# Kernel tuning notes

Hardware: AMD Instinct MI355X
Metric: run time of the kernel (lower is better)

Reference implementation:

```python
import jax, jax.numpy as jnp
import numpy as np
import math

E = 256      # emb_size
H = 4        # num_heads
D = E // H   # head_dim
EXPLORE_SCALE = 0.5
EXPLOIT_SCALE = 0.5
TEMP_MIN = 0.5
TEMP_MAX = 2.0


def setup_inputs() -> dict:
    key = jax.random.key(0)
    ks = jax.random.split(key, 12)
    B, S = 4, 2048
    his_emb = jax.random.normal(ks[0], (B, S, E), dtype=jnp.float32)
    src_key_padding_mask = jax.random.randint(ks[1], (B, S), 0, 2) > 0
    explore = jax.random.uniform(ks[2], (B, S), dtype=jnp.float32)
    exploit = jax.random.uniform(ks[3], (B, S), dtype=jnp.float32)
    scale = 1.0 / math.sqrt(E)
    Wq = jax.random.normal(ks[4], (E, E), dtype=jnp.float32) * scale
    bq = jnp.zeros((E,), dtype=jnp.float32)
    Wk = jax.random.normal(ks[5], (E, E), dtype=jnp.float32) * scale
    bk = jnp.zeros((E,), dtype=jnp.float32)
    Wv = jax.random.normal(ks[6], (E, E), dtype=jnp.float32) * scale
    bv = jnp.zeros((E,), dtype=jnp.float32)
    Wo = jax.random.normal(ks[7], (E, E), dtype=jnp.float32) * scale
    bo = jnp.zeros((E,), dtype=jnp.float32)
    return {"his_emb": his_emb, "src_key_padding_mask": src_key_padding_mask,
            "explore": explore, "exploit": exploit,
            "Wq": Wq, "bq": bq, "Wk": Wk, "bk": bk,
            "Wv": Wv, "bv": bv, "Wo": Wo, "bo": bo}


def reference(his_emb, src_key_padding_mask, explore, exploit,
              Wq, bq, Wk, bk, Wv, bv, Wo, bo):
    B, S, _ = his_emb.shape
    # projections -> [B, H, S, D]
    q = (his_emb @ Wq + bq).reshape(B, S, H, D).transpose(0, 2, 1, 3)
    k = (his_emb @ Wk + bk).reshape(B, S, H, D).transpose(0, 2, 1, 3)
    v = (his_emb @ Wv + bv).reshape(B, S, H, D).transpose(0, 2, 1, 3)
    logits = jnp.einsum('bhqd,bhkd->bhqk', q, k) / math.sqrt(D)
    attn_mask = src_key_padding_mask[:, None, None, :]  # [B,1,1,S] over keys
    logits = jnp.where(attn_mask, -1e16, logits)
    # per-query dynamic temperature
    temp = 1.0 + EXPLORE_SCALE * explore - EXPLOIT_SCALE * exploit  # [B,S]
    temp = jnp.clip(temp, TEMP_MIN, TEMP_MAX)
    temp = jnp.where(src_key_padding_mask, 1.0, temp)
    logits = logits / temp[:, None, :, None]
    probs = jax.nn.softmax(logits, axis=-1)
    probs = jnp.where(attn_mask, 0.0, probs)
    probs = probs / jnp.maximum(probs.sum(axis=-1, keepdims=True), 1e-8)
    out = jnp.einsum('bhqk,bhkd->bhqd', probs, v)
    out = out.transpose(0, 2, 1, 3).reshape(B, S, E)
    out = out @ Wo + bo
    return jnp.where(src_key_padding_mask[:, :, None], 0.0, out)
```

## Files before the change

kernel.cpp:

```cpp
#include <hip/hip_runtime.h>
#include <hip/hip_bf16.h>
#include <math.h>

#define B_ 4
#define S_ 2048
#define E_ 256
#define H_ 4
#define D_ 64
#define NROW (B_*S_)
#define NCH 4
#define CHK (S_/NCH)
#define FM 12.0f

typedef __attribute__((ext_vector_type(8))) short short8;
typedef __attribute__((ext_vector_type(4))) float floatx4;

__device__ __forceinline__ short f2bf(float f){
    union{float f; unsigned u;} x; x.f = f;
    unsigned r = x.u + 0x7fffu + ((x.u>>16)&1u);
    return (short)(r>>16);
}
__device__ __forceinline__ float bf2f(short s){
    union{unsigned u; float f;} x; x.u = ((unsigned)(unsigned short)s)<<16; return x.f;
}
__device__ __forceinline__ unsigned pk_trunc(float lo, float hi){
    return __builtin_amdgcn_perm(__float_as_uint(hi), __float_as_uint(lo), 0x07060302u);
}

__global__ __launch_bounds__(256) void convert_x(const float* __restrict__ X, short* __restrict__ Xb){
    int gid = blockIdx.x*256 + threadIdx.x;
    const float4* p = (const float4*)(X + (size_t)gid*8);
    float4 a = p[0], b = p[1];
    short8 o;
    o[0]=f2bf(a.x); o[1]=f2bf(a.y); o[2]=f2bf(a.z); o[3]=f2bf(a.w);
    o[4]=f2bf(b.x); o[5]=f2bf(b.y); o[6]=f2bf(b.z); o[7]=f2bf(b.w);
    *(short8*)(Xb + (size_t)gid*8) = o;
}

__global__ __launch_bounds__(256) void transpose_w(
    const float* __restrict__ W0, const float* __restrict__ W1,
    const float* __restrict__ W2, const float* __restrict__ W3,
    short* __restrict__ T0, short* __restrict__ T1,
    short* __restrict__ T2, short* __restrict__ T3)
{
    const float* W = blockIdx.y==0?W0: blockIdx.y==1?W1: blockIdx.y==2?W2:W3;
    short*       T = blockIdx.y==0?T0: blockIdx.y==1?T1: blockIdx.y==2?T2:T3;
    __shared__ float L[64][65];
    const int t = threadIdx.x;
    const int k0 = (blockIdx.x>>2)*64, n0 = (blockIdx.x&3)*64;
    {
        int r = t>>2, c0 = (t&3)*16;
        const float4* p = (const float4*)(W + (size_t)(k0+r)*E_ + n0 + c0);
        #pragma unroll
        for (int j=0;j<4;++j){
            float4 u = p[j];
            L[r][c0+4*j]=u.x; L[r][c0+4*j+1]=u.y; L[r][c0+4*j+2]=u.z; L[r][c0+4*j+3]=u.w;
        }
    }
    __syncthreads();
    {
        int n = t>>2, kk0 = (t&3)*16;
        short8 o0, o1;
        #pragma unroll
        for(int j=0;j<8;++j) o0[j] = f2bf(L[kk0+j][n]);
        #pragma unroll
        for(int j=0;j<8;++j) o1[j] = f2bf(L[kk0+8+j][n]);
        short* dst = T + (size_t)(n0+n)*E_ + k0 + kk0;
        *(short8*)dst = o0; *(short8*)(dst+8) = o1;
    }
}

__global__ __launch_bounds__(256) void qkv_gemm(
    const short* __restrict__ Xb,
    const short* __restrict__ Wtq, const float* __restrict__ bq,
    const short* __restrict__ Wtk, const float* __restrict__ bk,
    const short* __restrict__ Wtv, const float* __restrict__ bv,
    const int* __restrict__ mask,
    const float* __restrict__ explore, const float* __restrict__ exploit,
    short* __restrict__ Q, short* __restrict__ K, short* __restrict__ Vt)
{
    const int z = blockIdx.z;
    const short* Wt   = z==0?Wtq: z==1?Wtk:Wtv;
    const float* bias = z==0?bq:  z==1?bk:bv;

    __shared__ __align__(16) short As[64][72];
    __shared__ __align__(16) short Bs[64][72];

    const int t=threadIdx.x, w=t>>6, lane=t&63, ln=lane&15, quad=lane>>4;
    const int m0 = blockIdx.y*64, n0 = blockIdx.x*64;

    floatx4 acc[4] = {};
    for (int kt=0; kt<E_; kt+=64){
        __syncthreads();
        {
            int r=t>>2, c0=(t&3)*16;
            const uint4* pa = (const uint4*)(Xb + (size_t)(m0+r)*E_ + kt + c0);
            *(uint4*)&As[r][c0] = pa[0]; *(uint4*)&As[r][c0+8] = pa[1];
            const uint4* pb = (const uint4*)(Wt + (size_t)(n0+r)*E_ + kt + c0);
            *(uint4*)&Bs[r][c0] = pb[0]; *(uint4*)&Bs[r][c0+8] = pb[1];
        }
        __syncthreads();
        short8 a0 = *(const short8*)&As[w*16+ln][quad*8];
        short8 a1 = *(const short8*)&As[w*16+ln][32+quad*8];
        #pragma unroll
        for (int c=0;c<4;++c){
            short8 b0 = *(const short8*)&Bs[c*16+ln][quad*8];
            short8 b1 = *(const short8*)&Bs[c*16+ln][32+quad*8];
            acc[c] = __builtin_amdgcn_mfma_f32_16x16x32_bf16(a0,b0,acc[c],0,0,0);
            acc[c] = __builtin_amdgcn_mfma_f32_16x16x32_bf16(a1,b1,acc[c],0,0,0);
        }
    }
    if (z==0){
        float tscr[4];
        #pragma unroll
        for(int reg=0;reg<4;++reg){
            int row = m0 + w*16 + quad*4 + reg;
            float ex = explore[row], xp = exploit[row];
            float tmp = fminf(fmaxf(1.0f + 0.5f*ex - 0.5f*xp, 0.5f), 2.0f);
            tscr[reg] = mask[row] ? 0.125f : 1.0f/(8.0f*tmp);
        }
        #pragma unroll
        for(int c=0;c<4;++c){
            int colg = n0 + c*16 + ln;
            float bia = bias[colg];
            #pragma unroll
            for(int reg=0;reg<4;++reg){
                int row = m0 + w*16 + quad*4 + reg;
                Q[(size_t)row*E_ + colg] = f2bf((acc[c][reg] + bia)*tscr[reg]);
            }
        }
    } else if (z==1){
        #pragma unroll
        for(int c=0;c<4;++c){
            int colg = n0 + c*16 + ln;
            float bia = bias[colg];
            #pragma unroll
            for(int reg=0;reg<4;++reg){
                int row = m0 + w*16 + quad*4 + reg;
                K[(size_t)row*E_ + colg] = f2bf(acc[c][reg] + bia);
            }
        }
    } else {
        #pragma unroll
        for(int c=0;c<4;++c){
            int colg = n0 + c*16 + ln;
            int hx = colg>>6, d = colg&63;
            float bia = bias[colg];
            #pragma unroll
            for(int reg=0;reg<4;++reg){
                int row = m0 + w*16 + quad*4 + reg;
                int bb = row>>11, s = row&(S_-1);
                Vt[((size_t)((bb*H_+hx)*D_+d))*S_ + s] = f2bf(acc[c][reg] + bia);
            }
        }
    }
}

__global__ __launch_bounds__(256,4) void attn_mfma(
    const short* __restrict__ Qb, const short* __restrict__ Kb, const short* __restrict__ Vtb,
    const int* __restrict__ mask,
    short* __restrict__ OP, float* __restrict__ Lb)
{
    const int bh = blockIdx.z;
    const int b = bh>>2, h = bh&3;
    const int q0 = blockIdx.x*128;
    const int ck = blockIdx.y, k0 = ck*CHK;
    const int t=threadIdx.x, w=t>>6, lane=t&63, ln=lane&15, quad=lane>>4;

    __shared__ __align__(16) short Ks[64*64];
    __shared__ __align__(16) short Ps[4][32][72];
    __shared__ float mv[64];

    short8 qa[2][2];
    #pragma unroll
    for (int qh=0; qh<2; ++qh){
        const short* qr = Qb + (size_t)(b*S_ + q0 + w*32 + qh*16 + ln)*E_ + h*D_;
        qa[qh][0] = *(const short8*)(qr + quad*8);
        qa[qh][1] = *(const short8*)(qr + 32 + quad*8);
    }

    const int sr = t>>2, scc = (t&3)*2;
    short* kst0 = &Ks[sr*64 + ((scc  )^(sr&7))*8];
    short* kst1 = &Ks[sr*64 + ((scc+1)^(sr&7))*8];
    const short* kgl = Kb + (size_t)(b*S_ + sr)*E_ + h*D_ + scc*8;

    floatx4 of[2][4] = {};
    float lacc[2] = {0.f, 0.f};

    for (int kt=k0; kt<k0+CHK; kt+=64){
        __syncthreads();
        {
            const uint4* g = (const uint4*)(kgl + (size_t)kt*E_);
            *(uint4*)kst0 = g[0];
            *(uint4*)kst1 = g[1];
        }
        if (t<64) mv[t] = (mask[b*S_+kt+t] ? -1e30f : 0.0f) - FM;
        __syncthreads();

        #pragma unroll
        for (int c=0;c<4;++c){
            short8 ka0 = *(const short8*)&Ks[(c*16+ln)*64 + ((quad  )^(ln&7))*8];
            short8 ka1 = *(const short8*)&Ks[(c*16+ln)*64 + ((4+quad)^(ln&7))*8];
            float4 mvv = *(const float4*)&mv[c*16+quad*4];
            #pragma unroll
            for (int qh=0; qh<2; ++qh){
                floatx4 s = {};
                s = __builtin_amdgcn_mfma_f32_16x16x32_bf16(ka0, qa[qh][0], s, 0,0,0);
                s = __builtin_amdgcn_mfma_f32_16x16x32_bf16(ka1, qa[qh][1], s, 0,0,0);
                float p0 = __expf(s[0] + mvv.x);
                float p1 = __expf(s[1] + mvv.y);
                float p2 = __expf(s[2] + mvv.z);
                float p3 = __expf(s[3] + mvv.w);
                lacc[qh] += (p0+p1)+(p2+p3);
                uint2 pw; pw.x = pk_trunc(p0,p1); pw.y = pk_trunc(p2,p3);
                *(uint2*)&Ps[w][qh*16+ln][c*16+quad*4] = pw;
            }
        }

        #pragma unroll
        for (int half=0; half<2; ++half){
            short8 pa0 = *(const short8*)&Ps[w][ln]   [half*32 + quad*8];
            short8 pa1 = *(const short8*)&Ps[w][16+ln][half*32 + quad*8];
            #pragma unroll
            for (int dc=0; dc<4; ++dc){
                short8 vb = *(const short8*)(Vtb + ((size_t)(bh*D_ + dc*16+ln))*S_ + kt + half*32 + quad*8);
                of[0][dc] = __builtin_amdgcn_mfma_f32_16x16x32_bf16(pa0, vb, of[0][dc], 0,0,0);
                of[1][dc] = __builtin_amdgcn_mfma_f32_16x16x32_bf16(pa1, vb, of[1][dc], 0,0,0);
            }
        }
    }

    #pragma unroll
    for (int qh=0; qh<2; ++qh){
        float l = lacc[qh];
        l += __shfl_xor(l, 16);
        l += __shfl_xor(l, 32);
        #pragma unroll
        for (int dc=0; dc<4; ++dc){
            #pragma unroll
            for (int reg=0; reg<4; ++reg){
                int q = q0 + w*32 + qh*16 + quad*4 + reg;
                OP[((size_t)(ck*16 + bh)*S_ + q)*D_ + dc*16 + ln] = f2bf(of[qh][dc][reg]);
            }
        }
        if (quad==0)
            Lb[(size_t)(ck*16 + bh)*S_ + q0 + w*32 + qh*16 + ln] = l;
    }
}

__global__ __launch_bounds__(256) void combine(
    const short* __restrict__ OP, const float* __restrict__ Lb, short* __restrict__ CTXb)
{
    int gid = blockIdx.x*256 + threadIdx.x;
    #pragma unroll
    for (int i=0;i<4;++i){
        int idx = gid + i*524288;
        int e = idx & 255, row = idx >> 8;
        int bb = row >> 11, s = row & (S_-1);
        int hh = e >> 6, d = e & 63;
        int bh = bb*H_ + hh;
        float o = 0.f, l = 0.f;
        #pragma unroll
        for (int c=0;c<NCH;++c){
            o += bf2f(OP[((size_t)(c*16 + bh)*S_ + s)*D_ + d]);
            l += Lb[(size_t)(c*16 + bh)*S_ + s];
        }
        CTXb[idx] = f2bf(o / fmaxf(l, 1e-8f));
    }
}

__global__ __launch_bounds__(256) void out_gemm(
    const short* __restrict__ Ab, const short* __restrict__ Wto, const float* __restrict__ bo,
    const int* __restrict__ mask, float* __restrict__ out)
{
    __shared__ __align__(16) short As[64][72];
    __shared__ __align__(16) short Bs[64][72];
    const int t=threadIdx.x, w=t>>6, lane=t&63, ln=lane&15, quad=lane>>4;
    const int m0 = blockIdx.y*64, n0 = blockIdx.x*64;
    floatx4 acc[4] = {};
    for (int kt=0; kt<E_; kt+=64){
        __syncthreads();
        {
            int r=t>>2, c0=(t&3)*16;
            const uint4* pa = (const uint4*)(Ab + (size_t)(m0+r)*E_ + kt + c0);
            *(uint4*)&As[r][c0] = pa[0]; *(uint4*)&As[r][c0+8] = pa[1];
            const uint4* pb = (const uint4*)(Wto + (size_t)(n0+r)*E_ + kt + c0);
            *(uint4*)&Bs[r][c0] = pb[0]; *(uint4*)&Bs[r][c0+8] = pb[1];
        }
        __syncthreads();
        short8 a0 = *(const short8*)&As[w*16+ln][quad*8];
        short8 a1 = *(const short8*)&As[w*16+ln][32+quad*8];
        #pragma unroll
        for (int c=0;c<4;++c){
            short8 b0 = *(const short8*)&Bs[c*16+ln][quad*8];
            short8 b1 = *(const short8*)&Bs[c*16+ln][32+quad*8];
            acc[c] = __builtin_amdgcn_mfma_f32_16x16x32_bf16(a0,b0,acc[c],0,0,0);
            acc[c] = __builtin_amdgcn_mfma_f32_16x16x32_bf16(a1,b1,acc[c],0,0,0);
        }
    }
    #pragma unroll
    for(int c=0;c<4;++c){
        int colg = n0 + c*16 + ln;
        float bia = bo[colg];
        #pragma unroll
        for(int reg=0;reg<4;++reg){
            int row = m0 + w*16 + quad*4 + reg;
            out[(size_t)row*E_ + colg] = mask[row] ? 0.0f : (acc[c][reg] + bia);
        }
    }
}

extern "C" void kernel_launch(void* const* d_in, const int* in_sizes, int n_in,
                              void* d_out, int out_size, void* d_ws, size_t ws_size,
                              hipStream_t stream) {
    const float* his     = (const float*)d_in[0];
    const int*   mask    = (const int*)d_in[1];
    const float* explore = (const float*)d_in[2];
    const float* exploit = (const float*)d_in[3];
    const float* Wq = (const float*)d_in[4];
    const float* bq = (const float*)d_in[5];
    const float* Wk = (const float*)d_in[6];
    const float* bk = (const float*)d_in[7];
    const float* Wv = (const float*)d_in[8];
    const float* bv = (const float*)d_in[9];
    const float* Wo = (const float*)d_in[10];
    const float* bo = (const float*)d_in[11];

    char* ws = (char*)d_ws;
    const size_t NE2 = (size_t)NROW * E_ * 2;
    short* Wtq  = (short*)(ws);                    ws += E_*E_*2;
    short* Wtk  = (short*)(ws);                    ws += E_*E_*2;
    short* Wtv  = (short*)(ws);                    ws += E_*E_*2;
    short* Wto  = (short*)(ws);                    ws += E_*E_*2;
    short* Qb   = (short*)(ws);                    ws += NE2;
    short* Kb   = (short*)(ws);                    ws += NE2;
    short* Vtb  = (short*)(ws);                    ws += NE2;
    short* OP   = (short*)(ws);                    ws += (size_t)NCH*B_*H_*S_*D_*2;
    float* Lb   = (float*)(ws);                    ws += (size_t)NCH*B_*H_*S_*4;
    short* Xb   = OP;
    short* CTXb = Qb;

    convert_x<<<1024, 256, 0, stream>>>(his, Xb);
    transpose_w<<<dim3(16,4), 256, 0, stream>>>(Wq, Wk, Wv, Wo, Wtq, Wtk, Wtv, Wto);

    qkv_gemm<<<dim3(E_/64, NROW/64, 3), 256, 0, stream>>>(
        Xb, Wtq, bq, Wtk, bk, Wtv, bv, mask, explore, exploit, Qb, Kb, Vtb);

    attn_mfma<<<dim3(S_/128, NCH, B_*H_), 256, 0, stream>>>(
        Qb, Kb, Vtb, mask, OP, Lb);

    combine<<<2048, 256, 0, stream>>>(OP, Lb, CTXb);

    out_gemm<<<dim3(E_/64, NROW/64), 256, 0, stream>>>(CTXb, Wto, bo, mask, (float*)d_out);
}
```

Before: 152.1 us.

## Fuse input conversion and split-K combine into GEMMs; prefetch next tiles

Removes the separate convert_x and combine kernels. The QKV GEMM now reads fp32 input directly and converts it to bf16 while staging, and the output GEMM sums the four split-K partial outputs and normalises them inside its A-tile staging. All three GEMM/attention loops now issue register prefetches of the next K/V/X tiles before computing on the current shared-memory tile. This cuts two launches and an intermediate round trip through global memory, at the cost of more registers and redundant partial-sum reads across the output-GEMM column blocks.

```diff
diff --git a/kernel.cpp b/kernel.cpp
--- a/kernel.cpp
+++ b/kernel.cpp
@@ -25,16 +25,6 @@
 }
 __device__ __forceinline__ unsigned pk_trunc(float lo, float hi){
     return __builtin_amdgcn_perm(__float_as_uint(hi), __float_as_uint(lo), 0x07060302u);
-}
-
-__global__ __launch_bounds__(256) void convert_x(const float* __restrict__ X, short* __restrict__ Xb){
-    int gid = blockIdx.x*256 + threadIdx.x;
-    const float4* p = (const float4*)(X + (size_t)gid*8);
-    float4 a = p[0], b = p[1];
-    short8 o;
-    o[0]=f2bf(a.x); o[1]=f2bf(a.y); o[2]=f2bf(a.z); o[3]=f2bf(a.w);
-    o[4]=f2bf(b.x); o[5]=f2bf(b.y); o[6]=f2bf(b.z); o[7]=f2bf(b.w);
-    *(short8*)(Xb + (size_t)gid*8) = o;
 }
 
 __global__ __launch_bounds__(256) void transpose_w(
@@ -71,7 +61,7 @@
 }
 
 __global__ __launch_bounds__(256) void qkv_gemm(
-    const short* __restrict__ Xb,
+    const float* __restrict__ X,
     const short* __restrict__ Wtq, const float* __restrict__ bq,
     const short* __restrict__ Wtk, const float* __restrict__ bk,
     const short* __restrict__ Wtv, const float* __restrict__ bv,
@@ -88,18 +78,35 @@
 
     const int t=threadIdx.x, w=t>>6, lane=t&63, ln=lane&15, quad=lane>>4;
     const int m0 = blockIdx.y*64, n0 = blockIdx.x*64;
+    const int r = t>>2, c0 = (t&3)*16;
+    const float* xg = X  + (size_t)(m0+r)*E_ + c0;
+    const short* wg = Wt + (size_t)(n0+r)*E_ + c0;
+
+    float4 xa[4]; uint4 wb[2];
+    #pragma unroll
+    for (int j=0;j<4;++j) xa[j] = ((const float4*)xg)[j];
+    wb[0] = ((const uint4*)wg)[0]; wb[1] = ((const uint4*)wg)[1];
+
+    #define STAGE_QKV() do { \
+        short8 s0_, s1_; \
+        s0_[0]=f2bf(xa[0].x); s0_[1]=f2bf(xa[0].y); s0_[2]=f2bf(xa[0].z); s0_[3]=f2bf(xa[0].w); \
+        s0_[4]=f2bf(xa[1].x); s0_[5]=f2bf(xa[1].y); s0_[6]=f2bf(xa[1].z); s0_[7]=f2bf(xa[1].w); \
+        s1_[0]=f2bf(xa[2].x); s1_[1]=f2bf(xa[2].y); s1_[2]=f2bf(xa[2].z); s1_[3]=f2bf(xa[2].w); \
+        s1_[4]=f2bf(xa[3].x); s1_[5]=f2bf(xa[3].y); s1_[6]=f2bf(xa[3].z); s1_[7]=f2bf(xa[3].w); \
+        *(short8*)&As[r][c0] = s0_; *(short8*)&As[r][c0+8] = s1_; \
+        *(uint4*)&Bs[r][c0] = wb[0]; *(uint4*)&Bs[r][c0+8] = wb[1]; \
+    } while(0)
+
+    STAGE_QKV();
+    __syncthreads();
 
     floatx4 acc[4] = {};
     for (int kt=0; kt<E_; kt+=64){
-        __syncthreads();
-        {
-            int r=t>>2, c0=(t&3)*16;
-            const uint4* pa = (const uint4*)(Xb + (size_t)(m0+r)*E_ + kt + c0);
-            *(uint4*)&As[r][c0] = pa[0]; *(uint4*)&As[r][c0+8] = pa[1];
-            const uint4* pb = (const uint4*)(Wt + (size_t)(n0+r)*E_ + kt + c0);
-            *(uint4*)&Bs[r][c0] = pb[0]; *(uint4*)&Bs[r][c0+8] = pb[1];
-        }
-        __syncthreads();
+        int ktn = (kt+64 < E_) ? kt+64 : 0;
+        #pragma unroll
+        for (int j=0;j<4;++j) xa[j] = ((const float4*)(xg + ktn))[j];
+        wb[0] = ((const uint4*)(wg + ktn))[0]; wb[1] = ((const uint4*)(wg + ktn))[1];
+
         short8 a0 = *(const short8*)&As[w*16+ln][quad*8];
         short8 a1 = *(const short8*)&As[w*16+ln][32+quad*8];
         #pragma unroll
@@ -109,7 +116,11 @@
             acc[c] = __builtin_amdgcn_mfma_f32_16x16x32_bf16(a0,b0,acc[c],0,0,0);
             acc[c] = __builtin_amdgcn_mfma_f32_16x16x32_bf16(a1,b1,acc[c],0,0,0);
         }
-    }
+        __syncthreads();
+        STAGE_QKV();
+        __syncthreads();
+    }
+
     if (z==0){
         float tscr[4];
         #pragma unroll
@@ -183,19 +194,31 @@
     short* kst0 = &Ks[sr*64 + ((scc  )^(sr&7))*8];
     short* kst1 = &Ks[sr*64 + ((scc+1)^(sr&7))*8];
     const short* kgl = Kb + (size_t)(b*S_ + sr)*E_ + h*D_ + scc*8;
+    const short* vgl = Vtb + (size_t)bh*D_*S_;
 
     floatx4 of[2][4] = {};
     float lacc[2] = {0.f, 0.f};
 
+    {
+        const uint4* g = (const uint4*)(kgl + (size_t)k0*E_);
+        uint4 p0 = g[0], p1 = g[1];
+        *(uint4*)kst0 = p0; *(uint4*)kst1 = p1;
+        if (t<64) mv[t] = (mask[b*S_+k0+t] ? -1e30f : 0.0f) - FM;
+    }
+    __syncthreads();
+
     for (int kt=k0; kt<k0+CHK; kt+=64){
-        __syncthreads();
-        {
-            const uint4* g = (const uint4*)(kgl + (size_t)kt*E_);
-            *(uint4*)kst0 = g[0];
-            *(uint4*)kst1 = g[1];
-        }
-        if (t<64) mv[t] = (mask[b*S_+kt+t] ? -1e30f : 0.0f) - FM;
-        __syncthreads();
+        const int ktn = (kt+64 < k0+CHK) ? kt+64 : k0;
+
+        const uint4* gn = (const uint4*)(kgl + (size_t)ktn*E_);
+        uint4 nk0 = gn[0], nk1 = gn[1];
+
+        short8 vf[2][4];
+        #pragma unroll
+        for (int half=0; half<2; ++half)
+            #pragma unroll
+            for (int dc=0; dc<4; ++dc)
+                vf[half][dc] = *(const short8*)(vgl + (size_t)(dc*16+ln)*S_ + kt + half*32 + quad*8);
 
         #pragma unroll
         for (int c=0;c<4;++c){
@@ -223,11 +246,15 @@
             short8 pa1 = *(const short8*)&Ps[w][16+ln][half*32 + quad*8];
             #pragma unroll
             for (int dc=0; dc<4; ++dc){
-                short8 vb = *(const short8*)(Vtb + ((size_t)(bh*D_ + dc*16+ln))*S_ + kt + half*32 + quad*8);
-                of[0][dc] = __builtin_amdgcn_mfma_f32_16x16x32_bf16(pa0, vb, of[0][dc], 0,0,0);
-                of[1][dc] = __builtin_amdgcn_mfma_f32_16x16x32_bf16(pa1, vb, of[1][dc], 0,0,0);
-            }
-        }
+                of[0][dc] = __builtin_amdgcn_mfma_f32_16x16x32_bf16(pa0, vf[half][dc], of[0][dc], 0,0,0);
+                of[1][dc] = __builtin_amdgcn_mfma_f32_16x16x32_bf16(pa1, vf[half][dc], of[1][dc], 0,0,0);
+            }
+        }
+
+        __syncthreads();
+        *(uint4*)kst0 = nk0; *(uint4*)kst1 = nk1;
+        if (t<64) mv[t] = (mask[b*S_+ktn+t] ? -1e30f : 0.0f) - FM;
+        __syncthreads();
     }
 
     #pragma unroll
@@ -248,46 +275,60 @@
     }
 }
 
-__global__ __launch_bounds__(256) void combine(
-    const short* __restrict__ OP, const float* __restrict__ Lb, short* __restrict__ CTXb)
-{
-    int gid = blockIdx.x*256 + threadIdx.x;
-    #pragma unroll
-    for (int i=0;i<4;++i){
-        int idx = gid + i*524288;
-        int e = idx & 255, row = idx >> 8;
-        int bb = row >> 11, s = row & (S_-1);
-        int hh = e >> 6, d = e & 63;
-        int bh = bb*H_ + hh;
-        float o = 0.f, l = 0.f;
-        #pragma unroll
-        for (int c=0;c<NCH;++c){
-            o += bf2f(OP[((size_t)(c*16 + bh)*S_ + s)*D_ + d]);
-            l += Lb[(size_t)(c*16 + bh)*S_ + s];
-        }
-        CTXb[idx] = f2bf(o / fmaxf(l, 1e-8f));
-    }
-}
-
 __global__ __launch_bounds__(256) void out_gemm(
-    const short* __restrict__ Ab, const short* __restrict__ Wto, const float* __restrict__ bo,
+    const short* __restrict__ OP, const float* __restrict__ Lb,
+    const short* __restrict__ Wto, const float* __restrict__ bo,
     const int* __restrict__ mask, float* __restrict__ out)
 {
     __shared__ __align__(16) short As[64][72];
     __shared__ __align__(16) short Bs[64][72];
     const int t=threadIdx.x, w=t>>6, lane=t&63, ln=lane&15, quad=lane>>4;
     const int m0 = blockIdx.y*64, n0 = blockIdx.x*64;
+    const int r = t>>2, c0 = (t&3)*16;
+    const int row = m0 + r, bq = row>>11, s = row&(S_-1);
+    const short* wg = Wto + (size_t)(n0+r)*E_ + c0;
+
+    uint4 opk[NCH][2]; float lv[NCH]; uint4 wb[2];
+
+    #define LOAD_OUT(ktv) do { \
+        int h_ = (ktv)>>6, bh_ = bq*H_ + h_; \
+        _Pragma("unroll") \
+        for (int cc=0; cc<NCH; ++cc){ \
+            const uint4* p_ = (const uint4*)(OP + ((size_t)(cc*16 + bh_)*S_ + s)*D_ + c0); \
+            opk[cc][0] = p_[0]; opk[cc][1] = p_[1]; \
+            lv[cc] = Lb[(size_t)(cc*16 + bh_)*S_ + s]; \
+        } \
+        wb[0] = ((const uint4*)(wg + (ktv)))[0]; wb[1] = ((const uint4*)(wg + (ktv)))[1]; \
+    } while(0)
+
+    #define STAGE_OUT() do { \
+        float linv_ = 1.0f / fmaxf(lv[0]+lv[1]+lv[2]+lv[3], 1e-8f); \
+        short8 s0_, s1_; \
+        _Pragma("unroll") \
+        for (int j=0;j<8;++j){ \
+            float o_ = bf2f(((const short*)&opk[0][0])[j]) + bf2f(((const short*)&opk[1][0])[j]) \
+                     + bf2f(((const short*)&opk[2][0])[j]) + bf2f(((const short*)&opk[3][0])[j]); \
+            s0_[j] = f2bf(o_ * linv_); \
+        } \
+        _Pragma("unroll") \
+        for (int j=0;j<8;++j){ \
+            float o_ = bf2f(((const short*)&opk[0][1])[j]) + bf2f(((const short*)&opk[1][1])[j]) \
+                     + bf2f(((const short*)&opk[2][1])[j]) + bf2f(((const short*)&opk[3][1])[j]); \
+            s1_[j] = f2bf(o_ * linv_); \
+        } \
+        *(short8*)&As[r][c0] = s0_; *(short8*)&As[r][c0+8] = s1_; \
+        *(uint4*)&Bs[r][c0] = wb[0]; *(uint4*)&Bs[r][c0+8] = wb[1]; \
+    } while(0)
+
+    LOAD_OUT(0);
+    STAGE_OUT();
+    __syncthreads();
+
     floatx4 acc[4] = {};
     for (int kt=0; kt<E_; kt+=64){
-        __syncthreads();
-        {
-            int r=t>>2, c0=(t&3)*16;
-            const uint4* pa = (const uint4*)(Ab + (size_t)(m0+r)*E_ + kt + c0);
-            *(uint4*)&As[r][c0] = pa[0]; *(uint4*)&As[r][c0+8] = pa[1];
-            const uint4* pb = (const uint4*)(Wto + (size_t)(n0+r)*E_ + kt + c0);
-            *(uint4*)&Bs[r][c0] = pb[0]; *(uint4*)&Bs[r][c0+8] = pb[1];
-        }
-        __syncthreads();
+        int ktn = (kt+64 < E_) ? kt+64 : 0;
+        LOAD_OUT(ktn);
+
         short8 a0 = *(const short8*)&As[w*16+ln][quad*8];
         short8 a1 = *(const short8*)&As[w*16+ln][32+quad*8];
         #pragma unroll
@@ -297,15 +338,19 @@
             acc[c] = __builtin_amdgcn_mfma_f32_16x16x32_bf16(a0,b0,acc[c],0,0,0);
             acc[c] = __builtin_amdgcn_mfma_f32_16x16x32_bf16(a1,b1,acc[c],0,0,0);
         }
-    }
+        __syncthreads();
+        STAGE_OUT();
+        __syncthreads();
+    }
+
     #pragma unroll
     for(int c=0;c<4;++c){
         int colg = n0 + c*16 + ln;
         float bia = bo[colg];
         #pragma unroll
         for(int reg=0;reg<4;++reg){
-            int row = m0 + w*16 + quad*4 + reg;
-            out[(size_t)row*E_ + colg] = mask[row] ? 0.0f : (acc[c][reg] + bia);
+            int rowg = m0 + w*16 + quad*4 + reg;
+            out[(size_t)rowg*E_ + colg] = mask[rowg] ? 0.0f : (acc[c][reg] + bia);
         }
     }
 }
@@ -337,19 +382,14 @@
     short* Vtb  = (short*)(ws);                    ws += NE2;
     short* OP   = (short*)(ws);                    ws += (size_t)NCH*B_*H_*S_*D_*2;
     float* Lb   = (float*)(ws);                    ws += (size_t)NCH*B_*H_*S_*4;
-    short* Xb   = OP;
-    short* CTXb = Qb;
-
-    convert_x<<<1024, 256, 0, stream>>>(his, Xb);
+
     transpose_w<<<dim3(16,4), 256, 0, stream>>>(Wq, Wk, Wv, Wo, Wtq, Wtk, Wtv, Wto);
 
     qkv_gemm<<<dim3(E_/64, NROW/64, 3), 256, 0, stream>>>(
-        Xb, Wtq, bq, Wtk, bk, Wtv, bv, mask, explore, exploit, Qb, Kb, Vtb);
+        his, Wtq, bq, Wtk, bk, Wtv, bv, mask, explore, exploit, Qb, Kb, Vtb);
 
     attn_mfma<<<dim3(S_/128, NCH, B_*H_), 256, 0, stream>>>(
         Qb, Kb, Vtb, mask, OP, Lb);
 
-    combine<<<2048, 256, 0, stream>>>(OP, Lb, CTXb);
-
-    out_gemm<<<dim3(E_/64, NROW/64), 256, 0, stream>>>(CTXb, Wto, bo, mask, (float*)d_out);
-}
+    out_gemm<<<dim3(E_/64, NROW/64), 256, 0, stream>>>(OP, Lb, Wto, bo, mask, (float*)d_out);
+}
```

After: 170.5 us. 12.0% more time.

## Fuse input conversion and split-K combine into GEMMs, read K directly

Applied to the files above, without the earlier changes.

Removes the separate fp32-to-bf16 conversion kernel by converting the input while loading tiles inside the QKV GEMM. Removes the combine kernel by merging the split-key partial outputs and normalizing them inside the output GEMM's A-tile load. The attention kernel now reads K rows and mask values straight from global memory into registers instead of staging them through shared memory, which drops two barriers per tile. In exchange, the QKV GEMM reads fp32 X once per column block, the output GEMM recomputes the combine once per column block, and the K loads are less coalesced.

```diff
diff --git a/kernel.cpp b/kernel.cpp
--- a/kernel.cpp
+++ b/kernel.cpp
@@ -25,16 +25,6 @@
 }
 __device__ __forceinline__ unsigned pk_trunc(float lo, float hi){
     return __builtin_amdgcn_perm(__float_as_uint(hi), __float_as_uint(lo), 0x07060302u);
-}
-
-__global__ __launch_bounds__(256) void convert_x(const float* __restrict__ X, short* __restrict__ Xb){
-    int gid = blockIdx.x*256 + threadIdx.x;
-    const float4* p = (const float4*)(X + (size_t)gid*8);
-    float4 a = p[0], b = p[1];
-    short8 o;
-    o[0]=f2bf(a.x); o[1]=f2bf(a.y); o[2]=f2bf(a.z); o[3]=f2bf(a.w);
-    o[4]=f2bf(b.x); o[5]=f2bf(b.y); o[6]=f2bf(b.z); o[7]=f2bf(b.w);
-    *(short8*)(Xb + (size_t)gid*8) = o;
 }
 
 __global__ __launch_bounds__(256) void transpose_w(
@@ -71,7 +61,7 @@
 }
 
 __global__ __launch_bounds__(256) void qkv_gemm(
-    const short* __restrict__ Xb,
+    const float* __restrict__ X,
     const short* __restrict__ Wtq, const float* __restrict__ bq,
     const short* __restrict__ Wtk, const float* __restrict__ bk,
     const short* __restrict__ Wtv, const float* __restrict__ bv,
@@ -94,8 +84,14 @@
         __syncthreads();
         {
             int r=t>>2, c0=(t&3)*16;
-            const uint4* pa = (const uint4*)(Xb + (size_t)(m0+r)*E_ + kt + c0);
-            *(uint4*)&As[r][c0] = pa[0]; *(uint4*)&As[r][c0+8] = pa[1];
+            const float4* pa = (const float4*)(X + (size_t)(m0+r)*E_ + kt + c0);
+            short8 s0, s1;
+            float4 u;
+            u=pa[0]; s0[0]=f2bf(u.x); s0[1]=f2bf(u.y); s0[2]=f2bf(u.z); s0[3]=f2bf(u.w);
+            u=pa[1]; s0[4]=f2bf(u.x); s0[5]=f2bf(u.y); s0[6]=f2bf(u.z); s0[7]=f2bf(u.w);
+            u=pa[2]; s1[0]=f2bf(u.x); s1[1]=f2bf(u.y); s1[2]=f2bf(u.z); s1[3]=f2bf(u.w);
+            u=pa[3]; s1[4]=f2bf(u.x); s1[5]=f2bf(u.y); s1[6]=f2bf(u.z); s1[7]=f2bf(u.w);
+            *(short8*)&As[r][c0] = s0; *(short8*)&As[r][c0+8] = s1;
             const uint4* pb = (const uint4*)(Wt + (size_t)(n0+r)*E_ + kt + c0);
             *(uint4*)&Bs[r][c0] = pb[0]; *(uint4*)&Bs[r][c0+8] = pb[1];
         }
@@ -167,9 +163,7 @@
     const int ck = blockIdx.y, k0 = ck*CHK;
     const int t=threadIdx.x, w=t>>6, lane=t&63, ln=lane&15, quad=lane>>4;
 
-    __shared__ __align__(16) short Ks[64*64];
     __shared__ __align__(16) short Ps[4][32][72];
-    __shared__ float mv[64];
 
     short8 qa[2][2];
     #pragma unroll
@@ -179,38 +173,33 @@
         qa[qh][1] = *(const short8*)(qr + 32 + quad*8);
     }
 
-    const int sr = t>>2, scc = (t&3)*2;
-    short* kst0 = &Ks[sr*64 + ((scc  )^(sr&7))*8];
-    short* kst1 = &Ks[sr*64 + ((scc+1)^(sr&7))*8];
-    const short* kgl = Kb + (size_t)(b*S_ + sr)*E_ + h*D_ + scc*8;
+    const short* kbase = Kb + (size_t)(b*S_)*E_ + h*D_;
+    const short* vgl   = Vtb + (size_t)bh*D_*S_;
+    const int*   mbase = mask + b*S_;
 
     floatx4 of[2][4] = {};
     float lacc[2] = {0.f, 0.f};
 
     for (int kt=k0; kt<k0+CHK; kt+=64){
-        __syncthreads();
-        {
-            const uint4* g = (const uint4*)(kgl + (size_t)kt*E_);
-            *(uint4*)kst0 = g[0];
-            *(uint4*)kst1 = g[1];
-        }
-        if (t<64) mv[t] = (mask[b*S_+kt+t] ? -1e30f : 0.0f) - FM;
-        __syncthreads();
-
         #pragma unroll
         for (int c=0;c<4;++c){
-            short8 ka0 = *(const short8*)&Ks[(c*16+ln)*64 + ((quad  )^(ln&7))*8];
-            short8 ka1 = *(const short8*)&Ks[(c*16+ln)*64 + ((4+quad)^(ln&7))*8];
-            float4 mvv = *(const float4*)&mv[c*16+quad*4];
+            const short* kr = kbase + (size_t)(kt + c*16 + ln)*E_;
+            short8 ka0 = *(const short8*)(kr + quad*8);
+            short8 ka1 = *(const short8*)(kr + 32 + quad*8);
+            int4 mk = *(const int4*)(mbase + kt + c*16 + quad*4);
+            float mv0 = mk.x ? -1e30f : -FM;
+            float mv1 = mk.y ? -1e30f : -FM;
+            float mv2 = mk.z ? -1e30f : -FM;
+            float mv3 = mk.w ? -1e30f : -FM;
             #pragma unroll
             for (int qh=0; qh<2; ++qh){
                 floatx4 s = {};
                 s = __builtin_amdgcn_mfma_f32_16x16x32_bf16(ka0, qa[qh][0], s, 0,0,0);
                 s = __builtin_amdgcn_mfma_f32_16x16x32_bf16(ka1, qa[qh][1], s, 0,0,0);
-                float p0 = __expf(s[0] + mvv.x);
-                float p1 = __expf(s[1] + mvv.y);
-                float p2 = __expf(s[2] + mvv.z);
-                float p3 = __expf(s[3] + mvv.w);
+                float p0 = __expf(s[0] + mv0);
+                float p1 = __expf(s[1] + mv1);
+                float p2 = __expf(s[2] + mv2);
+                float p3 = __expf(s[3] + mv3);
                 lacc[qh] += (p0+p1)+(p2+p3);
                 uint2 pw; pw.x = pk_trunc(p0,p1); pw.y = pk_trunc(p2,p3);
                 *(uint2*)&Ps[w][qh*16+ln][c*16+quad*4] = pw;
@@ -223,7 +212,7 @@
             short8 pa1 = *(const short8*)&Ps[w][16+ln][half*32 + quad*8];
             #pragma unroll
             for (int dc=0; dc<4; ++dc){
-                short8 vb = *(const short8*)(Vtb + ((size_t)(bh*D_ + dc*16+ln))*S_ + kt + half*32 + quad*8);
+                short8 vb = *(const short8*)(vgl + (size_t)(dc*16+ln)*S_ + kt + half*32 + quad*8);
                 of[0][dc] = __builtin_amdgcn_mfma_f32_16x16x32_bf16(pa0, vb, of[0][dc], 0,0,0);
                 of[1][dc] = __builtin_amdgcn_mfma_f32_16x16x32_bf16(pa1, vb, of[1][dc], 0,0,0);
             }
@@ -248,42 +237,41 @@
     }
 }
 
-__global__ __launch_bounds__(256) void combine(
-    const short* __restrict__ OP, const float* __restrict__ Lb, short* __restrict__ CTXb)
-{
-    int gid = blockIdx.x*256 + threadIdx.x;
-    #pragma unroll
-    for (int i=0;i<4;++i){
-        int idx = gid + i*524288;
-        int e = idx & 255, row = idx >> 8;
-        int bb = row >> 11, s = row & (S_-1);
-        int hh = e >> 6, d = e & 63;
-        int bh = bb*H_ + hh;
-        float o = 0.f, l = 0.f;
-        #pragma unroll
-        for (int c=0;c<NCH;++c){
-            o += bf2f(OP[((size_t)(c*16 + bh)*S_ + s)*D_ + d]);
-            l += Lb[(size_t)(c*16 + bh)*S_ + s];
-        }
-        CTXb[idx] = f2bf(o / fmaxf(l, 1e-8f));
-    }
-}
-
 __global__ __launch_bounds__(256) void out_gemm(
-    const short* __restrict__ Ab, const short* __restrict__ Wto, const float* __restrict__ bo,
+    const short* __restrict__ OP, const float* __restrict__ Lb,
+    const short* __restrict__ Wto, const float* __restrict__ bo,
     const int* __restrict__ mask, float* __restrict__ out)
 {
     __shared__ __align__(16) short As[64][72];
     __shared__ __align__(16) short Bs[64][72];
     const int t=threadIdx.x, w=t>>6, lane=t&63, ln=lane&15, quad=lane>>4;
     const int m0 = blockIdx.y*64, n0 = blockIdx.x*64;
+    const int r = t>>2, c0 = (t&3)*16;
+    const int row = m0 + r, bq = row>>11, s = row&(S_-1);
+
     floatx4 acc[4] = {};
     for (int kt=0; kt<E_; kt+=64){
         __syncthreads();
         {
-            int r=t>>2, c0=(t&3)*16;
-            const uint4* pa = (const uint4*)(Ab + (size_t)(m0+r)*E_ + kt + c0);
-            *(uint4*)&As[r][c0] = pa[0]; *(uint4*)&As[r][c0+8] = pa[1];
+            int h = kt>>6, bh_ = bq*H_ + h;
+            float osum[16]; float lsum = 0.f;
+            #pragma unroll
+            for (int j=0;j<16;++j) osum[j] = 0.f;
+            #pragma unroll
+            for (int cc=0; cc<NCH; ++cc){
+                const uint4* p = (const uint4*)(OP + ((size_t)(cc*16 + bh_)*S_ + s)*D_ + c0);
+                uint4 u0 = p[0], u1 = p[1];
+                const short* sp0 = (const short*)&u0;
+                const short* sp1 = (const short*)&u1;
+                #pragma unroll
+                for (int j=0;j<8;++j){ osum[j] += bf2f(sp0[j]); osum[8+j] += bf2f(sp1[j]); }
+                lsum += Lb[(size_t)(cc*16 + bh_)*S_ + s];
+            }
+            float linv = 1.0f / fmaxf(lsum, 1e-8f);
+            short8 s0, s1;
+            #pragma unroll
+            for (int j=0;j<8;++j){ s0[j] = f2bf(osum[j]*linv); s1[j] = f2bf(osum[8+j]*linv); }
+            *(short8*)&As[r][c0] = s0; *(short8*)&As[r][c0+8] = s1;
             const uint4* pb = (const uint4*)(Wto + (size_t)(n0+r)*E_ + kt + c0);
             *(uint4*)&Bs[r][c0] = pb[0]; *(uint4*)&Bs[r][c0+8] = pb[1];
         }
@@ -304,8 +292,8 @@
         float bia = bo[colg];
         #pragma unroll
         for(int reg=0;reg<4;++reg){
-            int row = m0 + w*16 + quad*4 + reg;
-            out[(size_t)row*E_ + colg] = mask[row] ? 0.0f : (acc[c][reg] + bia);
+            int rowg = m0 + w*16 + quad*4 + reg;
+            out[(size_t)rowg*E_ + colg] = mask[rowg] ? 0.0f : (acc[c][reg] + bia);
         }
     }
 }
@@ -337,19 +325,14 @@
     short* Vtb  = (short*)(ws);                    ws += NE2;
     short* OP   = (short*)(ws);                    ws += (size_t)NCH*B_*H_*S_*D_*2;
     float* Lb   = (float*)(ws);                    ws += (size_t)NCH*B_*H_*S_*4;
-    short* Xb   = OP;
-    short* CTXb = Qb;
-
-    convert_x<<<1024, 256, 0, stream>>>(his, Xb);
+
     transpose_w<<<dim3(16,4), 256, 0, stream>>>(Wq, Wk, Wv, Wo, Wtq, Wtk, Wtv, Wto);
 
     qkv_gemm<<<dim3(E_/64, NROW/64, 3), 256, 0, stream>>>(
-        Xb, Wtq, bq, Wtk, bk, Wtv, bv, mask, explore, exploit, Qb, Kb, Vtb);
+        his, Wtq, bq, Wtk, bk, Wtv, bv, mask, explore, exploit, Qb, Kb, Vtb);
 
     attn_mfma<<<dim3(S_/128, NCH, B_*H_), 256, 0, stream>>>(
         Qb, Kb, Vtb, mask, OP, Lb);
 
-    combine<<<2048, 256, 0, stream>>>(OP, Lb, CTXb);
-
-    out_gemm<<<dim3(E_/64, NROW/64), 256, 0, stream>>>(CTXb, Wto, bo, mask, (float*)d_out);
-}
+    out_gemm<<<dim3(E_/64, NROW/64), 256, 0, stream>>>(OP, Lb, Wto, bo, mask, (float*)d_out);
+}
```

Measured after the change: 177.5 us. +16.7%, slower.
